# Kernel tuning notes

Hardware: AMD Instinct MI355X
Metric: run time of the kernel (lower is better)

The kernel has to match this reference:

```python
import jax, jax.numpy as jnp
import numpy as np

NEG_SLOPE = 0.01  # torch F.leaky_relu default

def _leaky(v):
    return jnp.where(v > 0, v, NEG_SLOPE * v)

def _gcn_conv(h, W, b, row, col, n_nodes):
    # PyG GCNConv with add_self_loops=True, symmetric normalization:
    # out = D^{-1/2} (A + I) D^{-1/2} (h @ W) + b,  deg includes self loop (+1)
    xw = h @ W                                            # [N, H]
    deg = jnp.zeros((n_nodes,), xw.dtype).at[col].add(1.0) + 1.0
    dis = jax.lax.rsqrt(deg)
    norm = dis[row] * dis[col]                            # [E]
    agg = jnp.zeros_like(xw).at[col].add(norm[:, None] * xw[row])
    agg = agg + xw * (1.0 / deg)[:, None]                 # self-loop term: dis_i^2 = 1/deg_i
    return agg + b

def setup_inputs() -> dict:
    key = jax.random.key(0)
    ks = jax.random.split(key, 16)
    N, E, EL = 100000, 1600000, 200000
    IN, H, EA = 256, 64, 8
    s = 0.05
    return {
        "x": jax.random.normal(ks[0], (N, IN), jnp.float32),
        "edge_index": jax.random.randint(ks[1], (2, E), 0, N, jnp.int64),
        "edge_label_index": jax.random.randint(ks[2], (2, EL), 0, N, jnp.int64),
        "edge_attr": jax.random.normal(ks[3], (EL, EA), jnp.float32),
        "W1": jax.random.normal(ks[4], (IN, 128), jnp.float32) * s,
        "b1": jnp.zeros((128,), jnp.float32),
        "W2": jax.random.normal(ks[5], (128, H), jnp.float32) * s,
        "b2": jnp.zeros((H,), jnp.float32),
        "Wg1": jax.random.normal(ks[6], (H, H), jnp.float32) * s,
        "bg1": jnp.zeros((H,), jnp.float32),
        "Wg2": jax.random.normal(ks[7], (H, H), jnp.float32) * s,
        "bg2": jnp.zeros((H,), jnp.float32),
        "Wp": jax.random.normal(ks[8], (2 * H + EA, 1), jnp.float32) * s,
        "bp": jnp.zeros((1,), jnp.float32),
    }

def reference(x, edge_index, edge_label_index, edge_attr,
              W1, b1, W2, b2, Wg1, bg1, Wg2, bg2, Wp, bp):
    n_nodes = x.shape[0]
    row, col = edge_index[0], edge_index[1]
    # preprocess MLP (dropout p=0.0 -> identity)
    h = _leaky(x @ W1 + b1)
    h = _leaky(h @ W2 + b2)
    # two GCN layers
    h = _leaky(_gcn_conv(h, Wg1, bg1, row, col, n_nodes))
    h = _leaky(_gcn_conv(h, Wg2, bg2, row, col, n_nodes))
    # edge scoring head: gather-concat-linear
    h_src = h[edge_label_index[0]]
    h_dst = h[edge_label_index[1]]
    combined = jnp.concatenate([h_src, h_dst, edge_attr], axis=1)
    out = (combined @ Wp + bp).reshape(-1)
    return (out, h)
```

## Files before the change

kernel.cpp:

```cpp
#include <hip/hip_runtime.h>
#include <hip/hip_bf16.h>

typedef __attribute__((ext_vector_type(8))) short bf16x8;
typedef __attribute__((ext_vector_type(4))) float f32x4;

#define BSHIFT 8
#define BW 256
#define NSTR 8
#define BCAP 768
#define LCAP 24
#define KEDGE 16

__device__ __forceinline__ float lk(float v) { return v > 0.f ? v : 0.01f * v; }

__device__ __forceinline__ short f2b(float v) {
  union { __hip_bfloat16 h; short s; } u;
  u.h = __float2bfloat16(v);
  return u.s;
}
__device__ __forceinline__ float loadF(const void* p, size_t i, int f32) {
  return f32 ? ((const float*)p)[i]
             : __bfloat162float(((const __hip_bfloat16*)p)[i]);
}
__device__ __forceinline__ void storeF(void* p, size_t i, int f32, float v) {
  if (f32) ((float*)p)[i] = v;
  else     ((__hip_bfloat16*)p)[i] = __float2bfloat16(v);
}
__device__ __forceinline__ int loadI(const int* p, size_t base, size_t e, int i64) {
  return i64 ? p[2 * (base + e)] : p[base + e];
}
__device__ __forceinline__ float blo(unsigned u) {
  union { unsigned u; float f; } c; c.u = u << 16; return c.f;
}
__device__ __forceinline__ float bhi(unsigned u) {
  union { unsigned u; float f; } c; c.u = u & 0xffff0000u; return c.f;
}

__global__ void detect_kernel(const unsigned short* __restrict__ x,
                              const int* __restrict__ ei, int* __restrict__ flags) {
  int t = threadIdx.x;
  unsigned short u = x[t];
  int ex = (u >> 7) & 0xFF;
  if (ex >= 0xC0) atomicOr(&flags[0], 1);
  if (t < 128 && ei[2 * t + 1] != 0) atomicOr(&flags[1], 1);
}

__global__ __launch_bounds__(64) void pack_all(const void* __restrict__ W1,
                                               const void* __restrict__ W2,
                                               const void* __restrict__ G1,
                                               const void* __restrict__ G2,
                                               __hip_bfloat16* __restrict__ P1,
                                               __hip_bfloat16* __restrict__ P2,
                                               __hip_bfloat16* __restrict__ PG1,
                                               __hip_bfloat16* __restrict__ PG2,
                                               const int* __restrict__ flags) {
  int f32 = flags[0] != 0;
  int b = blockIdx.x;
  const void* W; __hip_bfloat16* P; int KS, N, ks, ct;
  if (b < 64)      { W = W1; P = P1;  KS = 8; N = 128; int c = b;      ks = c & 7; ct = c >> 3; }
  else if (b < 80) { W = W2; P = P2;  KS = 4; N = 64;  int c = b - 64; ks = c & 3; ct = c >> 2; }
  else if (b < 88) { W = G1; P = PG1; KS = 2; N = 64;  int c = b - 80; ks = c & 1; ct = c >> 1; }
  else             { W = G2; P = PG2; KS = 2; N = 64;  int c = b - 88; ks = c & 1; ct = c >> 1; }
  int lane = threadIdx.x;
  int g = lane >> 4, m = lane & 15;
  size_t base = ((size_t)(ct * KS + ks) * 64 + (size_t)lane) * 8;
#pragma unroll
  for (int j = 0; j < 8; ++j)
    P[base + j] = __float2bfloat16(
        loadF(W, (size_t)(ks * 32 + g * 8 + j) * N + (size_t)(ct * 16 + m), f32));
}

template <int KS, int CT, int AMODE>
__global__ __launch_bounds__(256) void gemm_bt(const void* __restrict__ A,
                                               const __hip_bfloat16* __restrict__ Bp,
                                               const void* __restrict__ bias,
                                               void* __restrict__ Out, int out_bf16,
                                               __hip_bfloat16* __restrict__ Yout,
                                               const float* __restrict__ dinv,
                                               int M, int N, int act,
                                               const int* __restrict__ flags) {
  constexpr int K = KS * 32;
  constexpr int CPR = K / 8;
  __shared__ char tile[32 * K * 2];
  int f32 = AMODE ? (flags[0] != 0) : 0;
  int tid = threadIdx.x;
  int lane = tid & 63;
  int w = tid >> 6;
  int m = lane & 15, g = lane >> 4;
  int row0 = blockIdx.x << 5;

  bool done = false;
  if constexpr (AMODE) {
    if (f32) {
      constexpr int PP = K / 64;
      float4 sr[2 * PP];
#pragma unroll
      for (int j = 0; j < PP; ++j) {
        int q = j * 256 + tid;
        int r = q / CPR, pc = q - r * CPR;
        int gr = row0 + r; if (gr >= M) gr = M - 1;
        const float* src = (const float*)A + (size_t)gr * K + (size_t)pc * 8;
        sr[2 * j]     = *(const float4*)src;
        sr[2 * j + 1] = *(const float4*)(src + 4);
      }
#pragma unroll
      for (int j = 0; j < PP; ++j) {
        int q = j * 256 + tid;
        int r = q / CPR, pc = q - r * CPR;
        bf16x8 ov;
        ov[0] = f2b(sr[2 * j].x);     ov[1] = f2b(sr[2 * j].y);
        ov[2] = f2b(sr[2 * j].z);     ov[3] = f2b(sr[2 * j].w);
        ov[4] = f2b(sr[2 * j + 1].x); ov[5] = f2b(sr[2 * j + 1].y);
        ov[6] = f2b(sr[2 * j + 1].z); ov[7] = f2b(sr[2 * j + 1].w);
        *(bf16x8*)(tile + (size_t)r * (K * 2) + (size_t)((pc ^ (r & 7)) * 16)) = ov;
      }
      done = true;
    }
  }
  if (!done) {
    constexpr int PERW = 32 * CPR / 4;
#pragma unroll
    for (int i = 0; i < PERW; i += 64) {
      int p = w * PERW + i + lane;
      int r = p / CPR, pc = p - r * CPR;
      int gr = row0 + r; if (gr >= M) gr = M - 1;
      const char* src = (const char*)A + (size_t)gr * (K * 2) +
                        (size_t)((pc ^ (r & 7)) * 16);
      char* dst = tile + (size_t)(w * PERW + i) * 16;
      __builtin_amdgcn_global_load_lds(
          (const __attribute__((address_space(1))) void*)src,
          (__attribute__((address_space(3))) void*)dst, 16, 0, 0);
    }
  }
  __syncthreads();

  const __hip_bfloat16* bbase = Bp + ((size_t)(w * CT) * KS * 64 + (size_t)lane) * 8;
  f32x4 accs[2][CT];
#pragma unroll
  for (int tt = 0; tt < 2; ++tt)
#pragma unroll
    for (int cc = 0; cc < CT; ++cc) accs[tt][cc] = (f32x4){0, 0, 0, 0};

#pragma unroll
  for (int ks = 0; ks < KS; ++ks) {
    bf16x8 a[2];
#pragma unroll
    for (int tt = 0; tt < 2; ++tt) {
      int r = tt * 16 + m;
      int c = ks * 4 + g;
      a[tt] = *(const bf16x8*)(tile + (size_t)r * (K * 2) +
                               (size_t)((c ^ (r & 7)) * 16));
    }
    const __hip_bfloat16* bb = bbase + (size_t)ks * 64 * 8;
#pragma unroll
    for (int cc = 0; cc < CT; ++cc) {
      bf16x8 b = *(const bf16x8*)(bb + (size_t)cc * KS * 64 * 8);
#pragma unroll
      for (int tt = 0; tt < 2; ++tt)
        accs[tt][cc] = __builtin_amdgcn_mfma_f32_16x16x32_bf16(a[tt], b, accs[tt][cc], 0, 0, 0);
    }
  }

  float bv[CT];
#pragma unroll
  for (int cc = 0; cc < CT; ++cc)
    bv[cc] = bias ? loadF(bias, (size_t)((w * CT + cc) * 16 + m), flags[0] != 0) : 0.f;
#pragma unroll
  for (int tt = 0; tt < 2; ++tt) {
#pragma unroll
    for (int r = 0; r < 4; ++r) {
      int ro = row0 + tt * 16 + g * 4 + r;
      if (ro < M) {
        float di = Yout ? dinv[ro] : 0.f;
#pragma unroll
        for (int cc = 0; cc < CT; ++cc) {
          int col = (w * CT + cc) * 16 + m;
          float v = accs[tt][cc][r] + bv[cc];
          if (act) v = lk(v);
          if (Out) {
            if (out_bf16) ((__hip_bfloat16*)Out)[(size_t)ro * N + col] = __float2bfloat16(v);
            else          ((float*)Out)[(size_t)ro * N + col] = v;
          }
          if (Yout) Yout[(size_t)ro * N + col] = __float2bfloat16(v * di);
        }
      }
    }
  }
}

__global__ __launch_bounds__(256) void bin_kernel(const int* __restrict__ ei,
                                                  int* __restrict__ cur,
                                                  int2* __restrict__ rec,
                                                  int E, int NB,
                                                  const int* __restrict__ flags) {
  extern __shared__ int lds[];
  int* bcnt = lds;
  int* gbase = lds + NB;
  int2* bins = (int2*)(lds + 2 * NB);
  int i64 = flags[1] == 0;
  int stripe = __builtin_amdgcn_s_getreg(63508) & (NSTR - 1);
  int t = threadIdx.x;
  const int perRound = 256 * KEDGE;
  for (int base = blockIdx.x * perRound; base < E; base += gridDim.x * perRound) {
    for (int b = t; b < NB; b += 256) bcnt[b] = 0;
    __syncthreads();
#pragma unroll 1
    for (int k = 0; k < KEDGE; ++k) {
      int i = base + k * 256 + t;
      if (i < E) {
        int r, c;
        if (i64) {
          r = ((const int2*)ei)[i].x;
          c = ((const int2*)ei)[(size_t)E + i].x;
        } else {
          r = ei[i];
          c = ei[(size_t)E + i];
        }
        int b = c >> BSHIFT;
        int pos = atomicAdd(&bcnt[b], 1);
        if (pos < LCAP) {
          bins[b * LCAP + pos] = make_int2(r, c);
        } else {
          int bs = b * NSTR + stripe;
          int slot = atomicAdd(&cur[bs], 1);
          if (slot < BCAP) rec[(size_t)bs * BCAP + slot] = make_int2(r, c);
        }
      }
    }
    __syncthreads();
    for (int b = t; b < NB; b += 256) {
      int n = min(bcnt[b], LCAP);
      if (n > 0) gbase[b] = atomicAdd(&cur[b * NSTR + stripe], n);
    }
    __syncthreads();
    int lane = t & 63, w = t >> 6;
    for (int b = w; b < NB; b += 4) {
      int n = min(bcnt[b], LCAP);
      if (n == 0) continue;
      int gb = gbase[b];
      size_t sb = (size_t)(b * NSTR + stripe) * BCAP;
      if (lane < n && gb + lane < BCAP)
        rec[sb + gb + lane] = bins[b * LCAP + lane];
    }
    __syncthreads();
  }
}

__global__ __launch_bounds__(512) void place_kernel(const int2* __restrict__ rec,
                                                    const int* __restrict__ cur,
                                                    int* __restrict__ rowptr,
                                                    int* __restrict__ csr,
                                                    float* __restrict__ dinv, int Nn) {
  int b = blockIdx.x;
  int lo = b << BSHIFT;
  int t = threadIdx.x;
  __shared__ int cnt[BW];
  __shared__ int sc[BW];
  __shared__ int cursor[BW];
  __shared__ int red[512];
  int part = 0;
  for (int i = t; i < b * NSTR; i += 512) part += min(cur[i], BCAP);
  red[t] = part;
  if (t < BW) cnt[t] = 0;
  __syncthreads();
  for (int o = 256; o > 0; o >>= 1) {
    if (t < o) red[t] += red[t + o];
    __syncthreads();
  }
  int base = red[0];
#pragma unroll 1
  for (int s = 0; s < NSTR; ++s) {
    int n = min(cur[b * NSTR + s], BCAP);
    const int2* rp = rec + (size_t)(b * NSTR + s) * BCAP;
    for (int j = t; j < n; j += 512) atomicAdd(&cnt[rp[j].y - lo], 1);
  }
  __syncthreads();
  int v = 0;
  if (t < BW) { v = cnt[t]; sc[t] = v; }
  __syncthreads();
  for (int o = 1; o < BW; o <<= 1) {
    int a = (t >= o && t < BW) ? sc[t - o] : 0;
    __syncthreads();
    if (t < BW) sc[t] += a;
    __syncthreads();
  }
  if (t < BW) {
    int col = lo + t;
    if (col < Nn) {
      rowptr[col] = base + sc[t];
      dinv[col] = rsqrtf((float)v + 1.0f);
    }
    cursor[t] = base + sc[t] - v;
  }
  __syncthreads();
#pragma unroll 1
  for (int s = 0; s < NSTR; ++s) {
    int n = min(cur[b * NSTR + s], BCAP);
    const int2* rp = rec + (size_t)(b * NSTR + s) * BCAP;
    for (int j = t; j < n; j += 512) {
      int2 e = rp[j];
      int pos = atomicAdd(&cursor[e.y - lo], 1);
      csr[pos] = e.x;
    }
  }
}

__global__ __launch_bounds__(256) void gather_kernel(const __hip_bfloat16* __restrict__ y,
                                                     const int* __restrict__ csr,
                                                     const int* __restrict__ rowptr,
                                                     const float* __restrict__ dinv,
                                                     const void* __restrict__ bias,
                                                     void* __restrict__ outp, size_t obase,
                                                     int out_use_flag, int Nn,
                                                     float* __restrict__ ssrc,
                                                     float* __restrict__ sdst,
                                                     const void* __restrict__ Wp,
                                                     const int* __restrict__ flags) {
  int f32 = flags[0] != 0;
  int of32 = out_use_flag ? f32 : 0;
  int lane = threadIdx.x & 63;
  int w = (blockIdx.x * blockDim.x + threadIdx.x) >> 6;
  if (2 * w >= Nn) return;
  int half = lane >> 5;
  int hl = lane & 31;
  int hb = half << 5;
  int node = 2 * w + half;
  int alive = node < Nn;
  int nd = alive ? node : Nn - 1;
  int s = (nd == 0) ? 0 : rowptr[nd - 1];
  int e = rowptr[nd];
  if (!alive) e = s;
  const unsigned* yu = (const unsigned*)y;
  float p0a = 0, p1a = 0, p0b = 0, p1b = 0;
  float p0c = 0, p1c = 0, p0d = 0, p1d = 0;
  for (int base = s; base < e; base += 32) {
    int cnt = e - base; if (cnt > 32) cnt = 32;
    int rl = (base + hl < e) ? csr[base + hl] : 0;
    int j = 0;
    for (; j + 8 <= cnt; j += 8) {
      int r0 = __shfl(rl, hb + j + 0, 64);
      int r1 = __shfl(rl, hb + j + 1, 64);
      int r2 = __shfl(rl, hb + j + 2, 64);
      int r3 = __shfl(rl, hb + j + 3, 64);
      int r4 = __shfl(rl, hb + j + 4, 64);
      int r5 = __shfl(rl, hb + j + 5, 64);
      int r6 = __shfl(rl, hb + j + 6, 64);
      int r7 = __shfl(rl, hb + j + 7, 64);
      unsigned u0 = yu[(unsigned)r0 * 32u + hl];
      unsigned u1 = yu[(unsigned)r1 * 32u + hl];
      unsigned u2 = yu[(unsigned)r2 * 32u + hl];
      unsigned u3 = yu[(unsigned)r3 * 32u + hl];
      unsigned u4 = yu[(unsigned)r4 * 32u + hl];
      unsigned u5 = yu[(unsigned)r5 * 32u + hl];
      unsigned u6 = yu[(unsigned)r6 * 32u + hl];
      unsigned u7 = yu[(unsigned)r7 * 32u + hl];
      p0a += blo(u0); p1a += bhi(u0);
      p0b += blo(u1); p1b += bhi(u1);
      p0c += blo(u2); p1c += bhi(u2);
      p0d += blo(u3); p1d += bhi(u3);
      p0a += blo(u4); p1a += bhi(u4);
      p0b += blo(u5); p1b += bhi(u5);
      p0c += blo(u6); p1c += bhi(u6);
      p0d += blo(u7); p1d += bhi(u7);
    }
    for (; j + 4 <= cnt; j += 4) {
      int r0 = __shfl(rl, hb + j + 0, 64);
      int r1 = __shfl(rl, hb + j + 1, 64);
      int r2 = __shfl(rl, hb + j + 2, 64);
      int r3 = __shfl(rl, hb + j + 3, 64);
      unsigned u0 = yu[(unsigned)r0 * 32u + hl];
      unsigned u1 = yu[(unsigned)r1 * 32u + hl];
      unsigned u2 = yu[(unsigned)r2 * 32u + hl];
      unsigned u3 = yu[(unsigned)r3 * 32u + hl];
      p0a += blo(u0); p1a += bhi(u0);
      p0b += blo(u1); p1b += bhi(u1);
      p0c += blo(u2); p1c += bhi(u2);
      p0d += blo(u3); p1d += bhi(u3);
    }
    for (; j < cnt; ++j) {
      int r0 = __shfl(rl, hb + j, 64);
      unsigned u0 = yu[(unsigned)r0 * 32u + hl];
      p0a += blo(u0); p1a += bhi(u0);
    }
  }
  float acc0 = (p0a + p0b) + (p0c + p0d);
  float acc1 = (p1a + p1b) + (p1c + p1d);
  unsigned un = yu[(unsigned)nd * 32u + hl];
  acc0 += blo(un); acc1 += bhi(un);
  float di = dinv[nd];
  int f = hl * 2;
  float v0 = lk(di * acc0 + loadF(bias, (size_t)f, f32));
  float v1 = lk(di * acc1 + loadF(bias, (size_t)(f + 1), f32));
  if (alive) {
    if (of32) {
      *(float2*)((float*)outp + obase + (size_t)node * 64 + f) = make_float2(v0, v1);
    } else {
      union { unsigned u; unsigned short ss[2]; } pk;
      pk.ss[0] = (unsigned short)f2b(v0);
      pk.ss[1] = (unsigned short)f2b(v1);
      *(unsigned*)((__hip_bfloat16*)outp + obase + (size_t)node * 64 + f) = pk.u;
    }
  }
  if (ssrc) {
    float q1 = v0 * loadF(Wp, (size_t)f, f32) + v1 * loadF(Wp, (size_t)(f + 1), f32);
    float q2 = v0 * loadF(Wp, (size_t)(64 + f), f32) + v1 * loadF(Wp, (size_t)(65 + f), f32);
#pragma unroll
    for (int o = 16; o > 0; o >>= 1) {
      q1 += __shfl_down(q1, o, 64);
      q2 += __shfl_down(q2, o, 64);
    }
    if (hl == 0 && alive) { ssrc[node] = q1; sdst[node] = q2; }
  }
}

__global__ __launch_bounds__(256) void edge_head_kernel(void* __restrict__ dout,
                                                        const int* __restrict__ eli,
                                                        const void* __restrict__ ea,
                                                        const float* __restrict__ ssrc,
                                                        const float* __restrict__ sdst,
                                                        const void* __restrict__ Wp,
                                                        const void* __restrict__ bp,
                                                        int EL, const int* __restrict__ flags) {
  int f32 = flags[0] != 0;
  int i64 = flags[1] == 0;
  int tid = blockIdx.x * blockDim.x + threadIdx.x;
  if (tid >= EL) return;
  int s = loadI(eli, 0, (size_t)tid, i64);
  int d = loadI(eli, (size_t)EL, (size_t)tid, i64);
  float acc = ssrc[s] + sdst[d] + loadF(bp, 0, f32);
  if (f32) {
    const float* eap = (const float*)ea + (size_t)tid * 8;
    float4 u0 = *(const float4*)eap;
    float4 u1 = *(const float4*)(eap + 4);
    acc += u0.x * loadF(Wp, 128, 1) + u0.y * loadF(Wp, 129, 1) +
           u0.z * loadF(Wp, 130, 1) + u0.w * loadF(Wp, 131, 1) +
           u1.x * loadF(Wp, 132, 1) + u1.y * loadF(Wp, 133, 1) +
           u1.z * loadF(Wp, 134, 1) + u1.w * loadF(Wp, 135, 1);
  } else {
    bf16x8 u = *(const bf16x8*)((const __hip_bfloat16*)ea + (size_t)tid * 8);
#pragma unroll
    for (int j = 0; j < 8; ++j) {
      union { short s; __hip_bfloat16 h; } cv; cv.s = u[j];
      acc += __bfloat162float(cv.h) * loadF(Wp, (size_t)(128 + j), 0);
    }
  }
  storeF(dout, (size_t)tid, f32, acc);
}

extern "C" void kernel_launch(void* const* d_in, const int* in_sizes, int n_in,
                              void* d_out, int out_size, void* d_ws, size_t ws_size,
                              hipStream_t stream) {
  const void* x   = d_in[0];
  const int* ei   = (const int*)d_in[1];
  const int* eli  = (const int*)d_in[2];
  const void* ea  = d_in[3];
  const void* W1  = d_in[4];
  const void* b1  = d_in[5];
  const void* W2  = d_in[6];
  const void* b2  = d_in[7];
  const void* Wg1 = d_in[8];
  const void* bg1 = d_in[9];
  const void* Wg2 = d_in[10];
  const void* bg2 = d_in[11];
  const void* Wp  = d_in[12];
  const void* bp  = d_in[13];

  const int Nn = in_sizes[0] / 256;
  const int E  = in_sizes[1] / 2;
  const int EL = in_sizes[2] / 2;
  const int NB = (Nn + BW - 1) >> BSHIFT;

  char* ws = (char*)d_ws;
  size_t off = 0;
  auto take = [&](size_t bytes) -> char* {
    char* p = ws + off;
    off = (off + bytes + 255) & ~(size_t)255;
    return p;
  };
  int*   flags  = (int*)take(256);
  int*   cur    = (int*)take((size_t)NB * NSTR * 4);
  int*   rowptr = (int*)take((size_t)Nn * 4);
  float* dinv   = (float*)take((size_t)Nn * 4);
  float* ssrc   = (float*)take((size_t)Nn * 4);
  float* sdst   = (float*)take((size_t)Nn * 4);
  int*   csr    = (int*)take((size_t)E * 4);
  int2*  rec    = (int2*)take((size_t)NB * NSTR * BCAP * 8);
  __hip_bfloat16* pW1 = (__hip_bfloat16*)take(256 * 128 * 2);
  __hip_bfloat16* pW2 = (__hip_bfloat16*)take(128 * 64 * 2);
  __hip_bfloat16* pG1 = (__hip_bfloat16*)take(64 * 64 * 2);
  __hip_bfloat16* pG2 = (__hip_bfloat16*)take(64 * 64 * 2);
  char* regionA = take((size_t)Nn * 128 * 4);
  char* regionB = take((size_t)Nn * 64 * 4);
  __hip_bfloat16* h1 = (__hip_bfloat16*)regionA;
  __hip_bfloat16* y = (__hip_bfloat16*)(regionA + (size_t)Nn * 64 * 4);
  __hip_bfloat16* h2 = (__hip_bfloat16*)regionB;
  __hip_bfloat16* h3 = (__hip_bfloat16*)regionB;

  hipMemsetAsync(flags, 0, 256 + (((size_t)NB * NSTR * 4 + 255) & ~(size_t)255), stream);
  detect_kernel<<<1, 256, 0, stream>>>((const unsigned short*)x, ei, flags);

  pack_all<<<96, 64, 0, stream>>>(W1, W2, Wg1, Wg2, pW1, pW2, pG1, pG2, flags);

  const int ldsbytes = NB * (8 + LCAP * 8);
  const int nbin = (E + 256 * KEDGE - 1) / (256 * KEDGE);
  bin_kernel<<<nbin, 256, ldsbytes, stream>>>(ei, cur, rec, E, NB, flags);
  place_kernel<<<NB, 512, 0, stream>>>(rec, cur, rowptr, csr, dinv, Nn);

  const int tblocks = (Nn + 31) / 32;
  gemm_bt<8, 2, 1><<<tblocks, 256, 0, stream>>>(x, pW1, b1, h1, 1, nullptr, nullptr,
                                                Nn, 128, 1, flags);
  gemm_bt<4, 1, 0><<<tblocks, 256, 0, stream>>>(h1, pW2, b2, h2, 1, nullptr, nullptr,
                                                Nn, 64, 1, flags);

  const int gwaves = (Nn + 1) / 2;
  const int gblocks = (gwaves + 3) / 4;
  gemm_bt<2, 1, 0><<<tblocks, 256, 0, stream>>>(h2, pG1, nullptr, nullptr, 0, y, dinv,
                                                Nn, 64, 0, flags);
  gather_kernel<<<gblocks, 256, 0, stream>>>(y, csr, rowptr, dinv, bg1,
                                             h3, 0, 0, Nn,
                                             nullptr, nullptr, nullptr, flags);

  gemm_bt<2, 1, 0><<<tblocks, 256, 0, stream>>>(h3, pG2, nullptr, nullptr, 0, y, dinv,
                                                Nn, 64, 0, flags);
  gather_kernel<<<gblocks, 256, 0, stream>>>(y, csr, rowptr, dinv, bg2,
                                             d_out, (size_t)EL, 1, Nn,
                                             ssrc, sdst, Wp, flags);

  edge_head_kernel<<<(EL + 255) / 256, 256, 0, stream>>>(d_out, eli, ea, ssrc, sdst,
                                                         Wp, bp, EL, flags);
}
```

Measured before the change: 372.7 us.

## Fuse the two preprocess MLP GEMMs into one kernel keeping h1 in LDS

```diff
diff --git a/kernel.cpp b/kernel.cpp
--- a/kernel.cpp
+++ b/kernel.cpp
@@ -25,9 +25,6 @@
 __device__ __forceinline__ void storeF(void* p, size_t i, int f32, float v) {
   if (f32) ((float*)p)[i] = v;
   else     ((__hip_bfloat16*)p)[i] = __float2bfloat16(v);
-}
-__device__ __forceinline__ int loadI(const int* p, size_t base, size_t e, int i64) {
-  return i64 ? p[2 * (base + e)] : p[base + e];
 }
 __device__ __forceinline__ float blo(unsigned u) {
   union { unsigned u; float f; } c; c.u = u << 16; return c.f;
@@ -70,7 +67,149 @@
         loadF(W, (size_t)(ks * 32 + g * 8 + j) * N + (size_t)(ct * 16 + m), f32));
 }
 
-template <int KS, int CT, int AMODE>
+__global__ __launch_bounds__(256) void gemm_fused12(const void* __restrict__ A,
+                                                    const __hip_bfloat16* __restrict__ Bp1,
+                                                    const void* __restrict__ b1,
+                                                    const __hip_bfloat16* __restrict__ Bp2,
+                                                    const void* __restrict__ b2,
+                                                    __hip_bfloat16* __restrict__ Out,
+                                                    int M, const int* __restrict__ flags) {
+  constexpr int K1 = 256, CPR1 = K1 / 8;
+  __shared__ char xtile[32 * K1 * 2];
+  __shared__ char h1t[32 * 128 * 2];
+  int f32 = flags[0] != 0;
+  int tid = threadIdx.x;
+  int lane = tid & 63;
+  int w = tid >> 6;
+  int m = lane & 15, g = lane >> 4;
+  int row0 = blockIdx.x << 5;
+
+  if (f32) {
+    constexpr int PP = K1 / 64;
+    float4 sr[2 * PP];
+#pragma unroll
+    for (int j = 0; j < PP; ++j) {
+      int q = j * 256 + tid;
+      int r = q / CPR1, pc = q - r * CPR1;
+      int gr = row0 + r; if (gr >= M) gr = M - 1;
+      const float* src = (const float*)A + (size_t)gr * K1 + (size_t)pc * 8;
+      sr[2 * j]     = *(const float4*)src;
+      sr[2 * j + 1] = *(const float4*)(src + 4);
+    }
+#pragma unroll
+    for (int j = 0; j < PP; ++j) {
+      int q = j * 256 + tid;
+      int r = q / CPR1, pc = q - r * CPR1;
+      bf16x8 ov;
+      ov[0] = f2b(sr[2 * j].x);     ov[1] = f2b(sr[2 * j].y);
+      ov[2] = f2b(sr[2 * j].z);     ov[3] = f2b(sr[2 * j].w);
+      ov[4] = f2b(sr[2 * j + 1].x); ov[5] = f2b(sr[2 * j + 1].y);
+      ov[6] = f2b(sr[2 * j + 1].z); ov[7] = f2b(sr[2 * j + 1].w);
+      *(bf16x8*)(xtile + (size_t)r * (K1 * 2) + (size_t)((pc ^ (r & 7)) * 16)) = ov;
+    }
+  } else {
+    constexpr int PERW = 32 * CPR1 / 4;
+#pragma unroll
+    for (int i = 0; i < PERW; i += 64) {
+      int p = w * PERW + i + lane;
+      int r = p / CPR1, pc = p - r * CPR1;
+      int gr = row0 + r; if (gr >= M) gr = M - 1;
+      const char* src = (const char*)A + (size_t)gr * (K1 * 2) +
+                        (size_t)((pc ^ (r & 7)) * 16);
+      char* dst = xtile + (size_t)(w * PERW + i) * 16;
+      __builtin_amdgcn_global_load_lds(
+          (const __attribute__((address_space(1))) void*)src,
+          (__attribute__((address_space(3))) void*)dst, 16, 0, 0);
+    }
+  }
+  __syncthreads();
+
+  {
+    const __hip_bfloat16* bbase = Bp1 + ((size_t)(w * 2) * 8 * 64 + (size_t)lane) * 8;
+    f32x4 accs[2][2];
+#pragma unroll
+    for (int tt = 0; tt < 2; ++tt)
+#pragma unroll
+      for (int cc = 0; cc < 2; ++cc) accs[tt][cc] = (f32x4){0, 0, 0, 0};
+#pragma unroll
+    for (int ks = 0; ks < 8; ++ks) {
+      bf16x8 a[2];
+#pragma unroll
+      for (int tt = 0; tt < 2; ++tt) {
+        int r = tt * 16 + m;
+        int c = ks * 4 + g;
+        a[tt] = *(const bf16x8*)(xtile + (size_t)r * (K1 * 2) +
+                                 (size_t)((c ^ (r & 7)) * 16));
+      }
+      const __hip_bfloat16* bb = bbase + (size_t)ks * 64 * 8;
+#pragma unroll
+      for (int cc = 0; cc < 2; ++cc) {
+        bf16x8 b = *(const bf16x8*)(bb + (size_t)cc * 8 * 64 * 8);
+#pragma unroll
+        for (int tt = 0; tt < 2; ++tt)
+          accs[tt][cc] = __builtin_amdgcn_mfma_f32_16x16x32_bf16(a[tt], b, accs[tt][cc], 0, 0, 0);
+      }
+    }
+    float bv[2];
+#pragma unroll
+    for (int cc = 0; cc < 2; ++cc)
+      bv[cc] = loadF(b1, (size_t)((w * 2 + cc) * 16 + m), f32);
+#pragma unroll
+    for (int tt = 0; tt < 2; ++tt) {
+#pragma unroll
+      for (int r = 0; r < 4; ++r) {
+        int row = tt * 16 + g * 4 + r;
+#pragma unroll
+        for (int cc = 0; cc < 2; ++cc) {
+          float v = lk(accs[tt][cc][r] + bv[cc]);
+          int colb = ((w * 2 + cc) * 16 + m) * 2;
+          int ch = colb >> 4, off = colb & 15;
+          *(__hip_bfloat16*)(h1t + (size_t)row * 256 +
+                             (size_t)((ch ^ (row & 7)) * 16) + off) =
+              __float2bfloat16(v);
+        }
+      }
+    }
+  }
+  __syncthreads();
+
+  {
+    const __hip_bfloat16* bbase = Bp2 + ((size_t)w * 4 * 64 + (size_t)lane) * 8;
+    f32x4 accs[2];
+    accs[0] = (f32x4){0, 0, 0, 0};
+    accs[1] = (f32x4){0, 0, 0, 0};
+#pragma unroll
+    for (int ks = 0; ks < 4; ++ks) {
+      bf16x8 a[2];
+#pragma unroll
+      for (int tt = 0; tt < 2; ++tt) {
+        int r = tt * 16 + m;
+        int c = ks * 4 + g;
+        a[tt] = *(const bf16x8*)(h1t + (size_t)r * 256 +
+                                 (size_t)((c ^ (r & 7)) * 16));
+      }
+      const __hip_bfloat16* bb = bbase + (size_t)ks * 64 * 8;
+      bf16x8 b = *(const bf16x8*)bb;
+#pragma unroll
+      for (int tt = 0; tt < 2; ++tt)
+        accs[tt] = __builtin_amdgcn_mfma_f32_16x16x32_bf16(a[tt], b, accs[tt], 0, 0, 0);
+    }
+    float bv = loadF(b2, (size_t)(w * 16 + m), f32);
+#pragma unroll
+    for (int tt = 0; tt < 2; ++tt) {
+#pragma unroll
+      for (int r = 0; r < 4; ++r) {
+        int ro = row0 + tt * 16 + g * 4 + r;
+        if (ro < M) {
+          int col = w * 16 + m;
+          Out[(size_t)ro * 64 + col] = __float2bfloat16(lk(accs[tt][r] + bv));
+        }
+      }
+    }
+  }
+}
+
+template <int KS, int CT>
 __global__ __launch_bounds__(256) void gemm_bt(const void* __restrict__ A,
                                                const __hip_bfloat16* __restrict__ Bp,
                                                const void* __restrict__ bias,
@@ -82,42 +221,13 @@
   constexpr int K = KS * 32;
   constexpr int CPR = K / 8;
   __shared__ char tile[32 * K * 2];
-  int f32 = AMODE ? (flags[0] != 0) : 0;
   int tid = threadIdx.x;
   int lane = tid & 63;
   int w = tid >> 6;
   int m = lane & 15, g = lane >> 4;
   int row0 = blockIdx.x << 5;
 
-  bool done = false;
-  if constexpr (AMODE) {
-    if (f32) {
-      constexpr int PP = K / 64;
-      float4 sr[2 * PP];
-#pragma unroll
-      for (int j = 0; j < PP; ++j) {
-        int q = j * 256 + tid;
-        int r = q / CPR, pc = q - r * CPR;
-        int gr = row0 + r; if (gr >= M) gr = M - 1;
-        const float* src = (const float*)A + (size_t)gr * K + (size_t)pc * 8;
-        sr[2 * j]     = *(const float4*)src;
-        sr[2 * j + 1] = *(const float4*)(src + 4);
-      }
-#pragma unroll
-      for (int j = 0; j < PP; ++j) {
-        int q = j * 256 + tid;
-        int r = q / CPR, pc = q - r * CPR;
-        bf16x8 ov;
-        ov[0] = f2b(sr[2 * j].x);     ov[1] = f2b(sr[2 * j].y);
-        ov[2] = f2b(sr[2 * j].z);     ov[3] = f2b(sr[2 * j].w);
-        ov[4] = f2b(sr[2 * j + 1].x); ov[5] = f2b(sr[2 * j + 1].y);
-        ov[6] = f2b(sr[2 * j + 1].z); ov[7] = f2b(sr[2 * j + 1].w);
-        *(bf16x8*)(tile + (size_t)r * (K * 2) + (size_t)((pc ^ (r & 7)) * 16)) = ov;
-      }
-      done = true;
-    }
-  }
-  if (!done) {
+  {
     constexpr int PERW = 32 * CPR / 4;
 #pragma unroll
     for (int i = 0; i < PERW; i += 64) {
@@ -161,10 +271,11 @@
     }
   }
 
+  int f32 = flags[0] != 0;
   float bv[CT];
 #pragma unroll
   for (int cc = 0; cc < CT; ++cc)
-    bv[cc] = bias ? loadF(bias, (size_t)((w * CT + cc) * 16 + m), flags[0] != 0) : 0.f;
+    bv[cc] = bias ? loadF(bias, (size_t)((w * CT + cc) * 16 + m), f32) : 0.f;
 #pragma unroll
   for (int tt = 0; tt < 2; ++tt) {
 #pragma unroll
@@ -425,8 +536,14 @@
   int i64 = flags[1] == 0;
   int tid = blockIdx.x * blockDim.x + threadIdx.x;
   if (tid >= EL) return;
-  int s = loadI(eli, 0, (size_t)tid, i64);
-  int d = loadI(eli, (size_t)EL, (size_t)tid, i64);
+  int s, d;
+  if (i64) {
+    s = ((const int2*)eli)[tid].x;
+    d = ((const int2*)eli)[(size_t)EL + tid].x;
+  } else {
+    s = eli[tid];
+    d = eli[(size_t)EL + tid];
+  }
   float acc = ssrc[s] + sdst[d] + loadF(bp, 0, f32);
   if (f32) {
     const float* eap = (const float*)ea + (size_t)tid * 8;
@@ -491,7 +608,6 @@
   __hip_bfloat16* pG2 = (__hip_bfloat16*)take(64 * 64 * 2);
   char* regionA = take((size_t)Nn * 128 * 4);
   char* regionB = take((size_t)Nn * 64 * 4);
-  __hip_bfloat16* h1 = (__hip_bfloat16*)regionA;
   __hip_bfloat16* y = (__hip_bfloat16*)(regionA + (size_t)Nn * 64 * 4);
   __hip_bfloat16* h2 = (__hip_bfloat16*)regionB;
   __hip_bfloat16* h3 = (__hip_bfloat16*)regionB;
@@ -507,21 +623,18 @@
   place_kernel<<<NB, 512, 0, stream>>>(rec, cur, rowptr, csr, dinv, Nn);
 
   const int tblocks = (Nn + 31) / 32;
-  gemm_bt<8, 2, 1><<<tblocks, 256, 0, stream>>>(x, pW1, b1, h1, 1, nullptr, nullptr,
-                                                Nn, 128, 1, flags);
-  gemm_bt<4, 1, 0><<<tblocks, 256, 0, stream>>>(h1, pW2, b2, h2, 1, nullptr, nullptr,
-                                                Nn, 64, 1, flags);
+  gemm_fused12<<<tblocks, 256, 0, stream>>>(x, pW1, b1, pW2, b2, h2, Nn, flags);
 
   const int gwaves = (Nn + 1) / 2;
   const int gblocks = (gwaves + 3) / 4;
-  gemm_bt<2, 1, 0><<<tblocks, 256, 0, stream>>>(h2, pG1, nullptr, nullptr, 0, y, dinv,
-                                                Nn, 64, 0, flags);
+  gemm_bt<2, 1><<<tblocks, 256, 0, stream>>>(h2, pG1, nullptr, nullptr, 0, y, dinv,
+                                             Nn, 64, 0, flags);
   gather_kernel<<<gblocks, 256, 0, stream>>>(y, csr, rowptr, dinv, bg1,
                                              h3, 0, 0, Nn,
                                              nullptr, nullptr, nullptr, flags);
 
-  gemm_bt<2, 1, 0><<<tblocks, 256, 0, stream>>>(h3, pG2, nullptr, nullptr, 0, y, dinv,
-                                                Nn, 64, 0, flags);
+  gemm_bt<2, 1><<<tblocks, 256, 0, stream>>>(h3, pG2, nullptr, nullptr, 0, y, dinv,
+                                             Nn, 64, 0, flags);
   gather_kernel<<<gblocks, 256, 0, stream>>>(y, csr, rowptr, dinv, bg2,
                                              d_out, (size_t)EL, 1, Nn,
                                              ssrc, sdst, Wp, flags);
```

Measured after the change: 361.6 us. -3.0%, faster.
